# Performance work log

Hardware: AMD Instinct MI355X
Metric: run time of the kernel (lower is better)

## Reference

```python
import jax, jax.numpy as jnp
import numpy as np

N = 10000       # nodes
E = 200000      # node pairs (edges) in rel_dict
R = 400000      # relation instances
F_IN = 128
F_OUT = 64


def setup_inputs() -> dict:
    key = jax.random.key(0)
    ks = jax.random.split(key, 8)
    x = jax.random.normal(ks[0], (N, F_IN), dtype=jnp.float32)
    rel = jax.random.normal(ks[1], (R, F_IN), dtype=jnp.float32)
    adj = jax.random.uniform(ks[2], (N, N), dtype=jnp.float32)
    edge_pairs = jax.random.randint(ks[3], (E, 2), 0, N, dtype=jnp.int32)
    rel_seg = jax.random.randint(ks[4], (R,), 0, E, dtype=jnp.int32)
    # Conv1d(in, out, kernel_size=1, bias=False) == Linear: weight [out, in]
    W = jax.random.normal(ks[5], (F_OUT, F_IN), dtype=jnp.float32) * 0.1
    w_rel = jax.random.normal(ks[6], (F_IN,), dtype=jnp.float32) * 0.1
    bias = jnp.zeros((F_OUT,), dtype=jnp.float32)
    return {"x": x, "rel": rel, "adj": adj, "edge_pairs": edge_pairs,
            "rel_seg": rel_seg, "W": W, "w_rel": w_rel, "bias": bias}


def reference(x, rel, adj, edge_pairs, rel_seg, W, w_rel, bias):
    # node transform: [N, F_OUT]
    seq_fts = x @ W.T
    # per-relation scalar: [R]
    fts_rel = rel @ w_rel
    # segment-mean per edge (vectorized form of the rel_dict loop)
    sums = jax.ops.segment_sum(fts_rel, rel_seg, num_segments=E)
    cnts = jax.ops.segment_sum(jnp.ones_like(fts_rel), rel_seg, num_segments=E)
    edge_means = sums / jnp.maximum(cnts, 1.0)  # [E]
    # symmetric scatter into dense logits [N, N]
    e1, e2 = edge_pairs[:, 0], edge_pairs[:, 1]
    logits = jnp.zeros_like(adj)
    logits = logits.at[e1, e2].set(edge_means).at[e2, e1].set(edge_means)
    # masked-ish softmax over rows, then sparse-weighted aggregation
    coefs = jax.nn.softmax(jax.nn.sigmoid(logits) + adj, axis=1)  # [N, N]
    # dropout is a no-op in eval mode (training=False)
    ret = coefs @ seq_fts + bias  # [N, F_OUT]
    return jax.nn.elu(ret)        # concat=True
```

## Files before the change

kernel.cpp:

```cpp
#include <hip/hip_runtime.h>
#include <math.h>

#define NN   10000
#define EE   200000
#define RR   400000
#define FIN  128
#define FOUT 64
#define NK   10048

#define HASH_BITS 20
#define HSIZE (1u << HASH_BITS)
#define HMASK (HSIZE - 1u)
#define ROWCAP 256

typedef __bf16 bf16x8 __attribute__((ext_vector_type(8)));
typedef __bf16 bf16x4 __attribute__((ext_vector_type(4)));
typedef float  f32x4  __attribute__((ext_vector_type(4)));

#define O_SUMS   0
#define O_CNTS   (O_SUMS + EE)
#define O_ROWCNT (O_CNTS + EE)
#define O_HKEY   (O_ROWCNT + NN)
#define O_HPRIO  (O_HKEY + HSIZE)
#define O_SEQT   (O_HPRIO + HSIZE)
#define ZERO_WORDS (O_SEQT + (FOUT * NK) / 2)
#define O_SEQ    ZERO_WORDS
#define O_NUMP   (O_SEQ + NN * FOUT)
#define O_SP     (O_NUMP + 8 * NN * FOUT)
#define O_PAIRS  (O_SP + 8 * NN)

__global__ __launch_bounds__(256) void k_zero(f32x4* __restrict__ p, int n4) {
    int gid = blockIdx.x * 256 + threadIdx.x;
    if (gid < n4) p[gid] = (f32x4){0.f, 0.f, 0.f, 0.f};
}

__global__ __launch_bounds__(256) void k_seqfts(const float* __restrict__ x,
                                                const float* __restrict__ W,
                                                float* __restrict__ seq,
                                                __bf16* __restrict__ seqT) {
    __shared__ float Wt[FIN][FOUT + 1];
    __shared__ float xs[FIN][16 + 1];
    int t = threadIdx.x;
    for (int e = t; e < FOUT * FIN; e += 256) {
        int c = e >> 7, k = e & 127;
        Wt[k][c] = W[e];
    }
    int row0 = blockIdx.x * 16;
    for (int e = t; e < 16 * FIN; e += 256) {
        int r = e >> 7, k = e & 127;
        int gr = row0 + r;
        xs[k][r] = (gr < NN) ? x[(size_t)gr * FIN + k] : 0.f;
    }
    __syncthreads();
    int col = t & 63;
    int rg  = t >> 6;
    float acc[4] = {0.f, 0.f, 0.f, 0.f};
    for (int k = 0; k < FIN; ++k) {
        float w = Wt[k][col];
        #pragma unroll
        for (int i = 0; i < 4; ++i) acc[i] += w * xs[k][rg * 4 + i];
    }
    #pragma unroll
    for (int i = 0; i < 4; ++i) {
        int gr = row0 + rg * 4 + i;
        if (gr < NN) {
            seq[(size_t)gr * FOUT + col] = acc[i];
            seqT[(size_t)col * NK + gr] = (__bf16)acc[i];
        }
    }
}

__device__ __forceinline__ unsigned hash_cell(unsigned cell) {
    return (cell * 2654435761u) >> (32 - HASH_BITS);
}
__device__ __forceinline__ void entry_ij(const int* ep, int e, int& i, int& j, int& k) {
    k = (e < EE) ? e : e - EE;
    int a = ep[2 * k], b = ep[2 * k + 1];
    if (e < EE) { i = a; j = b; } else { i = b; j = a; }
}

#define BM 64
#define BK 64
#define KSPLIT 8
#define NCHUNK 157
#define CPK ((NCHUNK + KSPLIT - 1) / KSPLIT)
#define MAINB (NCHUNK * KSPLIT)
#define ILV   11
#define MRB   (ILV * MAINB)
#define SCATAB ((2 * EE + 255) / 256)
#define GRID_MR (MRB + SCATAB)
#define LDAP (BK + 8)

__global__ __launch_bounds__(256) void k_mainrel(const float* __restrict__ adj,
                                                 const __bf16* __restrict__ seqT,
                                                 const float* __restrict__ rel,
                                                 const float* __restrict__ wrel,
                                                 const int* __restrict__ rseg,
                                                 const int* __restrict__ ep,
                                                 float* __restrict__ sums,
                                                 float* __restrict__ cnts,
                                                 unsigned* __restrict__ hkey,
                                                 unsigned* __restrict__ hprio,
                                                 float* __restrict__ Nump,
                                                 float* __restrict__ Sp) {
    __shared__ __bf16 As[2][BM][LDAP];
    __shared__ __bf16 Bs[2][FOUT][LDAP];
    int t   = threadIdx.x;
    int bid = blockIdx.x;

    if (bid >= MRB) {
        int e = (bid - MRB) * 256 + t;
        if (e >= 2 * EE) return;
        int i, j, k;
        entry_ij(ep, e, i, j, k);
        unsigned cell = (unsigned)i * NN + (unsigned)j;
        unsigned keyv = cell + 1u;
        unsigned h = hash_cell(cell);
        while (true) {
            unsigned old = atomicCAS(&hkey[h], 0u, keyv);
            if (old == 0u || old == keyv) break;
            h = (h + 1u) & HMASK;
        }
        atomicMax(&hprio[h], (unsigned)(e + 1));
        return;
    }

    if (bid % ILV) {
        int relb = bid - bid / ILV - 1;
        int lane = t & 31;
        f32x4 w = *(const f32x4*)(wrel + lane * 4);
        #pragma unroll
        for (int it = 0; it < 4; ++it) {
            int row = relb * 32 + it * 8 + (t >> 5);
            if (row < RR) {
                f32x4 v = *(const f32x4*)(rel + (size_t)row * FIN + lane * 4);
                float s = v.x * w.x + v.y * w.y + v.z * w.z + v.w * w.w;
                #pragma unroll
                for (int off = 16; off >= 1; off >>= 1) s += __shfl_xor(s, off, 64);
                if (lane == 0) {
                    int seg = rseg[row];
                    atomicAdd(&sums[seg], s);
                    atomicAdd(&cnts[seg], 1.0f);
                }
            }
        }
        return;
    }

    int mi   = bid / ILV;
    int rowc = mi % NCHUNK;
    int ks   = mi / NCHUNK;
    int row0 = rowc * BM;
    int c0   = ks * CPK;
    int c1   = min(NCHUNK, c0 + CPK);
    int w  = t >> 6, l = t & 63;
    int lr = l & 15, lk = l >> 4;
    int sr = t >> 4;
    int sk = (t & 15) * 4;
    int bc = t >> 3;
    int bk = (t & 7) * 8;

    f32x4 acc[4];
    #pragma unroll
    for (int n = 0; n < 4; ++n) acc[n] = (f32x4){0.f, 0.f, 0.f, 0.f};
    float rs[4] = {0.f, 0.f, 0.f, 0.f};

    f32x4  pva[4];
    bf16x8 pvb0, pvb1;

#define LOADC(CH)                                                              \
    {                                                                          \
        int k0_ = (CH) * BK;                                                   \
        _Pragma("unroll")                                                      \
        for (int e2 = 0; e2 < 4; ++e2) {                                       \
            int gr = row0 + sr + e2 * 16;                                      \
            int gk = k0_ + sk;                                                 \
            bool ok = (gr < NN) && (gk < NN);                                  \
            pva[e2] = ok ? *(const f32x4*)(adj + (size_t)gr * NN + gk)         \
                         : (f32x4){0.f, 0.f, 0.f, 0.f};                        \
        }                                                                      \
        pvb0 = *(const bf16x8*)(seqT + (size_t)bc * NK + k0_ + bk);            \
        pvb1 = *(const bf16x8*)(seqT + (size_t)(bc + 32) * NK + k0_ + bk);     \
    }

    LOADC(c0);
    int p = 0;
    for (int ch = c0; ch < c1; ++ch) {
        *(bf16x8*)&Bs[p][bc][bk]      = pvb0;
        *(bf16x8*)&Bs[p][bc + 32][bk] = pvb1;
        bool okk = (ch * BK + sk < NN);
        #pragma unroll
        for (int e2 = 0; e2 < 4; ++e2) {
            bool ok = okk && (row0 + sr + e2 * 16 < NN);
            float w0 = ok ? __expf(pva[e2].x + 0.5f) : 0.f;
            float w1 = ok ? __expf(pva[e2].y + 0.5f) : 0.f;
            float w2 = ok ? __expf(pva[e2].z + 0.5f) : 0.f;
            float w3 = ok ? __expf(pva[e2].w + 0.5f) : 0.f;
            bf16x4 bv = { (__bf16)w0, (__bf16)w1, (__bf16)w2, (__bf16)w3 };
            *(bf16x4*)&As[p][sr + e2 * 16][sk] = bv;
            rs[e2] += w0 + w1 + w2 + w3;
        }
        if (ch + 1 < c1) LOADC(ch + 1);
        __syncthreads();
        #pragma unroll
        for (int kss = 0; kss < 2; ++kss) {
            bf16x8 a = *(const bf16x8*)&As[p][w * 16 + lr][kss * 32 + lk * 8];
            #pragma unroll
            for (int n = 0; n < 4; ++n) {
                bf16x8 b = *(const bf16x8*)&Bs[p][n * 16 + lr][kss * 32 + lk * 8];
                acc[n] = __builtin_amdgcn_mfma_f32_16x16x32_bf16(a, b, acc[n], 0, 0, 0);
            }
        }
        p ^= 1;
    }
#undef LOADC

    #pragma unroll
    for (int e = 0; e < 4; ++e) {
        float pp = rs[e];
        pp += __shfl_xor(pp, 1, 64);
        pp += __shfl_xor(pp, 2, 64);
        pp += __shfl_xor(pp, 4, 64);
        pp += __shfl_xor(pp, 8, 64);
        int r = e * 16 + sr;
        if ((t & 15) == 0 && row0 + r < NN)
            Sp[(size_t)ks * NN + row0 + r] = pp;
    }
    #pragma unroll
    for (int n = 0; n < 4; ++n) {
        #pragma unroll
        for (int r = 0; r < 4; ++r) {
            int grow = row0 + w * 16 + lk * 4 + r;
            if (grow < NN)
                Nump[(size_t)ks * NN * FOUT + (size_t)grow * FOUT + n * 16 + lr]
                    = acc[n][r];
        }
    }
}

__global__ __launch_bounds__(256) void k_scatB(const int* __restrict__ ep,
                                               const float* __restrict__ sums,
                                               const float* __restrict__ cnts,
                                               const unsigned* __restrict__ hkey,
                                               const unsigned* __restrict__ hprio,
                                               const float* __restrict__ adj,
                                               int* __restrict__ rowcnt,
                                               uint2* __restrict__ pairs) {
    int e = blockIdx.x * 256 + threadIdx.x;
    if (e >= 2 * EE) return;
    int i, j, k;
    entry_ij(ep, e, i, j, k);
    unsigned cell = (unsigned)i * NN + (unsigned)j;
    unsigned keyv = cell + 1u;
    unsigned h = hash_cell(cell);
    while (hkey[h] != keyv) h = (h + 1u) & HMASK;
    if (hprio[h] == (unsigned)(e + 1)) {
        float v   = sums[k] / fmaxf(cnts[k], 1.0f);
        float sg  = 1.f / (1.f + __expf(-v));
        float aij = adj[(size_t)i * NN + j];
        float dw  = __expf(aij + sg) - __expf(aij + 0.5f);
        if (dw != 0.f) {
            int pos = atomicAdd(&rowcnt[i], 1);
            if (pos < ROWCAP)
                pairs[(size_t)i * ROWCAP + pos] =
                    make_uint2((unsigned)j, __float_as_uint(dw));
        }
    }
}

__global__ __launch_bounds__(256) void k_rowupd(const float* __restrict__ Nump,
                                                const float* __restrict__ Sp,
                                                const int* __restrict__ rowcnt,
                                                const uint2* __restrict__ pairs,
                                                const float* __restrict__ seq,
                                                const float* __restrict__ bias,
                                                float* __restrict__ out) {
    int t = threadIdx.x;
    int i = blockIdx.x * 4 + (t >> 6);
    if (i >= NN) return;
    int c = t & 63;
    float acc = 0.f, sb = 0.f;
    #pragma unroll
    for (int ks = 0; ks < 8; ++ks) {
        acc += Nump[(size_t)ks * NN * FOUT + (size_t)i * FOUT + c];
        sb  += Sp[(size_t)ks * NN + i];
    }
    int cnt = min(rowcnt[i], ROWCAP);
    float sdw = 0.f;
    const uint2* pr = pairs + (size_t)i * ROWCAP;
    #pragma unroll 4
    for (int e = 0; e < cnt; ++e) {
        uint2 pk = pr[e];
        float d  = __uint_as_float(pk.y);
        acc += d * seq[(size_t)pk.x * FOUT + c];
        sdw += d;
    }
    float v = acc / (sb + sdw) + bias[c];
    out[(size_t)i * FOUT + c] = (v > 0.f) ? v : expm1f(v);
}

extern "C" void kernel_launch(void* const* d_in, const int* in_sizes, int n_in,
                              void* d_out, int out_size, void* d_ws, size_t ws_size,
                              hipStream_t stream) {
    const float* x    = (const float*)d_in[0];
    const float* rel  = (const float*)d_in[1];
    const float* adj  = (const float*)d_in[2];
    const int*   ep   = (const int*)d_in[3];
    const int*   rseg = (const int*)d_in[4];
    const float* W    = (const float*)d_in[5];
    const float* wrel = (const float*)d_in[6];
    const float* bias = (const float*)d_in[7];
    float* out = (float*)d_out;

    float* ws = (float*)d_ws;
    float*    sums   = ws + O_SUMS;
    float*    cnts   = ws + O_CNTS;
    int*      rowcnt = (int*)(ws + O_ROWCNT);
    unsigned* hkey   = (unsigned*)(ws + O_HKEY);
    unsigned* hprio  = (unsigned*)(ws + O_HPRIO);
    __bf16*   seqT   = (__bf16*)(ws + O_SEQT);
    float*    seq    = ws + O_SEQ;
    float*    Nump   = ws + O_NUMP;
    float*    Sp     = ws + O_SP;
    uint2*    pairs  = (uint2*)(ws + O_PAIRS);

    int n4 = ZERO_WORDS / 4;
    k_zero<<<(n4 + 255) / 256, 256, 0, stream>>>((f32x4*)d_ws, n4);
    k_seqfts<<<NN / 16, 256, 0, stream>>>(x, W, seq, seqT);
    k_mainrel<<<GRID_MR, 256, 0, stream>>>(adj, seqT, rel, wrel, rseg, ep,
                                           sums, cnts, hkey, hprio, Nump, Sp);
    k_scatB<<<SCATAB, 256, 0, stream>>>(ep, sums, cnts, hkey, hprio, adj,
                                        rowcnt, pairs);
    k_rowupd<<<(NN + 3) / 4, 256, 0, stream>>>(Nump, Sp, rowcnt, pairs,
                                               seq, bias, out);
}
```

Baseline: 268.7 us.

## Restructure fused main kernel to per-wave register-only MFMA strips without LDS

```diff
diff --git a/kernel.cpp b/kernel.cpp
--- a/kernel.cpp
+++ b/kernel.cpp
@@ -14,7 +14,6 @@
 #define ROWCAP 256
 
 typedef __bf16 bf16x8 __attribute__((ext_vector_type(8)));
-typedef __bf16 bf16x4 __attribute__((ext_vector_type(4)));
 typedef float  f32x4  __attribute__((ext_vector_type(4)));
 
 #define O_SUMS   0
@@ -79,37 +78,113 @@
     if (e < EE) { i = a; j = b; } else { i = b; j = a; }
 }
 
-#define BM 64
 #define BK 64
 #define KSPLIT 8
 #define NCHUNK 157
-#define CPK ((NCHUNK + KSPLIT - 1) / KSPLIT)
-#define MAINB (NCHUNK * KSPLIT)
-#define ILV   11
-#define MRB   (ILV * MAINB)
-#define SCATAB ((2 * EE + 255) / 256)
-#define GRID_MR (MRB + SCATAB)
-#define LDAP (BK + 8)
-
-__global__ __launch_bounds__(256) void k_mainrel(const float* __restrict__ adj,
-                                                 const __bf16* __restrict__ seqT,
-                                                 const float* __restrict__ rel,
-                                                 const float* __restrict__ wrel,
-                                                 const int* __restrict__ rseg,
-                                                 const int* __restrict__ ep,
-                                                 float* __restrict__ sums,
-                                                 float* __restrict__ cnts,
-                                                 unsigned* __restrict__ hkey,
-                                                 unsigned* __restrict__ hprio,
-                                                 float* __restrict__ Nump,
-                                                 float* __restrict__ Sp) {
-    __shared__ __bf16 As[2][BM][LDAP];
-    __shared__ __bf16 Bs[2][FOUT][LDAP];
+#define CPK 20
+#define NSTRIP (NN / 16)
+#define MAINW (NSTRIP * KSPLIT)
+#define RELW  (RR / 16)
+#define HASHW ((2 * EE + 63) / 64)
+#define TOTW  (MAINW + RELW + HASHW)
+#define GRID_MR ((TOTW + 3) / 4)
+
+__global__ __launch_bounds__(256, 4) void k_mainrel(const float* __restrict__ adj,
+                                                    const __bf16* __restrict__ seqT,
+                                                    const float* __restrict__ rel,
+                                                    const float* __restrict__ wrel,
+                                                    const int* __restrict__ rseg,
+                                                    const int* __restrict__ ep,
+                                                    float* __restrict__ sums,
+                                                    float* __restrict__ cnts,
+                                                    unsigned* __restrict__ hkey,
+                                                    unsigned* __restrict__ hprio,
+                                                    float* __restrict__ Nump,
+                                                    float* __restrict__ Sp) {
     int t   = threadIdx.x;
-    int bid = blockIdx.x;
-
-    if (bid >= MRB) {
-        int e = (bid - MRB) * 256 + t;
+    int wid = blockIdx.x * 4 + (t >> 6);
+    int l   = t & 63;
+
+    if (wid < MAINW) {
+        int strip = wid % NSTRIP;
+        int ks    = wid / NSTRIP;
+        int row0  = strip * 16;
+        int c0 = ks * CPK, c1 = min(NCHUNK, c0 + CPK);
+        int lr = l & 15, lk = l >> 4;
+        const float*  arow  = adj  + (size_t)(row0 + lr) * NN;
+        const __bf16* bbase = seqT + (size_t)lr * NK;
+
+        f32x4 acc[4];
+        #pragma unroll
+        for (int n = 0; n < 4; ++n) acc[n] = (f32x4){0.f, 0.f, 0.f, 0.f};
+        float rs = 0.f;
+
+        for (int ch = c0; ch < c1; ++ch) {
+            int k0 = ch * BK;
+            #pragma unroll
+            for (int h = 0; h < 2; ++h) {
+                int gk = k0 + h * 32 + lk * 8;
+                f32x4 a0 = (f32x4){-1e9f, -1e9f, -1e9f, -1e9f};
+                f32x4 a1 = a0;
+                if (gk < NN) {
+                    a0 = *(const f32x4*)(arow + gk);
+                    a1 = *(const f32x4*)(arow + gk + 4);
+                }
+                float w0 = __expf(a0.x + 0.5f);
+                float w1 = __expf(a0.y + 0.5f);
+                float w2 = __expf(a0.z + 0.5f);
+                float w3 = __expf(a0.w + 0.5f);
+                float w4 = __expf(a1.x + 0.5f);
+                float w5 = __expf(a1.y + 0.5f);
+                float w6 = __expf(a1.z + 0.5f);
+                float w7 = __expf(a1.w + 0.5f);
+                rs += ((w0 + w1) + (w2 + w3)) + ((w4 + w5) + (w6 + w7));
+                bf16x8 af = { (__bf16)w0, (__bf16)w1, (__bf16)w2, (__bf16)w3,
+                              (__bf16)w4, (__bf16)w5, (__bf16)w6, (__bf16)w7 };
+                const __bf16* bp = bbase + gk;
+                #pragma unroll
+                for (int n = 0; n < 4; ++n) {
+                    bf16x8 b = *(const bf16x8*)(bp + (size_t)n * 16 * NK);
+                    acc[n] = __builtin_amdgcn_mfma_f32_16x16x32_bf16(af, b, acc[n], 0, 0, 0);
+                }
+            }
+        }
+        rs += __shfl_xor(rs, 16, 64);
+        rs += __shfl_xor(rs, 32, 64);
+        if (lk == 0) Sp[(size_t)ks * NN + row0 + lr] = rs;
+        float* nout = Nump + (size_t)ks * NN * FOUT;
+        #pragma unroll
+        for (int n = 0; n < 4; ++n) {
+            #pragma unroll
+            for (int r = 0; r < 4; ++r)
+                nout[(size_t)(row0 + lk * 4 + r) * FOUT + n * 16 + lr] = acc[n][r];
+        }
+        return;
+    }
+
+    if (wid < MAINW + RELW) {
+        int rw   = wid - MAINW;
+        int lane = l & 31;
+        int half = l >> 5;
+        f32x4 wv = *(const f32x4*)(wrel + lane * 4);
+        #pragma unroll
+        for (int it = 0; it < 8; ++it) {
+            int row = rw * 16 + it * 2 + half;
+            f32x4 v = *(const f32x4*)(rel + (size_t)row * FIN + lane * 4);
+            float s = v.x * wv.x + v.y * wv.y + v.z * wv.z + v.w * wv.w;
+            #pragma unroll
+            for (int off = 16; off >= 1; off >>= 1) s += __shfl_xor(s, off, 64);
+            if (lane == 0) {
+                int seg = rseg[row];
+                atomicAdd(&sums[seg], s);
+                atomicAdd(&cnts[seg], 1.0f);
+            }
+        }
+        return;
+    }
+
+    {
+        int e = (wid - MAINW - RELW) * 64 + l;
         if (e >= 2 * EE) return;
         int i, j, k;
         entry_ij(ep, e, i, j, k);
@@ -122,119 +197,6 @@
             h = (h + 1u) & HMASK;
         }
         atomicMax(&hprio[h], (unsigned)(e + 1));
-        return;
-    }
-
-    if (bid % ILV) {
-        int relb = bid - bid / ILV - 1;
-        int lane = t & 31;
-        f32x4 w = *(const f32x4*)(wrel + lane * 4);
-        #pragma unroll
-        for (int it = 0; it < 4; ++it) {
-            int row = relb * 32 + it * 8 + (t >> 5);
-            if (row < RR) {
-                f32x4 v = *(const f32x4*)(rel + (size_t)row * FIN + lane * 4);
-                float s = v.x * w.x + v.y * w.y + v.z * w.z + v.w * w.w;
-                #pragma unroll
-                for (int off = 16; off >= 1; off >>= 1) s += __shfl_xor(s, off, 64);
-                if (lane == 0) {
-                    int seg = rseg[row];
-                    atomicAdd(&sums[seg], s);
-                    atomicAdd(&cnts[seg], 1.0f);
-                }
-            }
-        }
-        return;
-    }
-
-    int mi   = bid / ILV;
-    int rowc = mi % NCHUNK;
-    int ks   = mi / NCHUNK;
-    int row0 = rowc * BM;
-    int c0   = ks * CPK;
-    int c1   = min(NCHUNK, c0 + CPK);
-    int w  = t >> 6, l = t & 63;
-    int lr = l & 15, lk = l >> 4;
-    int sr = t >> 4;
-    int sk = (t & 15) * 4;
-    int bc = t >> 3;
-    int bk = (t & 7) * 8;
-
-    f32x4 acc[4];
-    #pragma unroll
-    for (int n = 0; n < 4; ++n) acc[n] = (f32x4){0.f, 0.f, 0.f, 0.f};
-    float rs[4] = {0.f, 0.f, 0.f, 0.f};
-
-    f32x4  pva[4];
-    bf16x8 pvb0, pvb1;
-
-#define LOADC(CH)                                                              \
-    {                                                                          \
-        int k0_ = (CH) * BK;                                                   \
-        _Pragma("unroll")                                                      \
-        for (int e2 = 0; e2 < 4; ++e2) {                                       \
-            int gr = row0 + sr + e2 * 16;                                      \
-            int gk = k0_ + sk;                                                 \
-            bool ok = (gr < NN) && (gk < NN);                                  \
-            pva[e2] = ok ? *(const f32x4*)(adj + (size_t)gr * NN + gk)         \
-                         : (f32x4){0.f, 0.f, 0.f, 0.f};                        \
-        }                                                                      \
-        pvb0 = *(const bf16x8*)(seqT + (size_t)bc * NK + k0_ + bk);            \
-        pvb1 = *(const bf16x8*)(seqT + (size_t)(bc + 32) * NK + k0_ + bk);     \
-    }
-
-    LOADC(c0);
-    int p = 0;
-    for (int ch = c0; ch < c1; ++ch) {
-        *(bf16x8*)&Bs[p][bc][bk]      = pvb0;
-        *(bf16x8*)&Bs[p][bc + 32][bk] = pvb1;
-        bool okk = (ch * BK + sk < NN);
-        #pragma unroll
-        for (int e2 = 0; e2 < 4; ++e2) {
-            bool ok = okk && (row0 + sr + e2 * 16 < NN);
-            float w0 = ok ? __expf(pva[e2].x + 0.5f) : 0.f;
-            float w1 = ok ? __expf(pva[e2].y + 0.5f) : 0.f;
-            float w2 = ok ? __expf(pva[e2].z + 0.5f) : 0.f;
-            float w3 = ok ? __expf(pva[e2].w + 0.5f) : 0.f;
-            bf16x4 bv = { (__bf16)w0, (__bf16)w1, (__bf16)w2, (__bf16)w3 };
-            *(bf16x4*)&As[p][sr + e2 * 16][sk] = bv;
-            rs[e2] += w0 + w1 + w2 + w3;
-        }
-        if (ch + 1 < c1) LOADC(ch + 1);
-        __syncthreads();
-        #pragma unroll
-        for (int kss = 0; kss < 2; ++kss) {
-            bf16x8 a = *(const bf16x8*)&As[p][w * 16 + lr][kss * 32 + lk * 8];
-            #pragma unroll
-            for (int n = 0; n < 4; ++n) {
-                bf16x8 b = *(const bf16x8*)&Bs[p][n * 16 + lr][kss * 32 + lk * 8];
-                acc[n] = __builtin_amdgcn_mfma_f32_16x16x32_bf16(a, b, acc[n], 0, 0, 0);
-            }
-        }
-        p ^= 1;
-    }
-#undef LOADC
-
-    #pragma unroll
-    for (int e = 0; e < 4; ++e) {
-        float pp = rs[e];
-        pp += __shfl_xor(pp, 1, 64);
-        pp += __shfl_xor(pp, 2, 64);
-        pp += __shfl_xor(pp, 4, 64);
-        pp += __shfl_xor(pp, 8, 64);
-        int r = e * 16 + sr;
-        if ((t & 15) == 0 && row0 + r < NN)
-            Sp[(size_t)ks * NN + row0 + r] = pp;
-    }
-    #pragma unroll
-    for (int n = 0; n < 4; ++n) {
-        #pragma unroll
-        for (int r = 0; r < 4; ++r) {
-            int grow = row0 + w * 16 + lk * 4 + r;
-            if (grow < NN)
-                Nump[(size_t)ks * NN * FOUT + (size_t)grow * FOUT + n * 16 + lr]
-                    = acc[n][r];
-        }
     }
 }
 
@@ -329,8 +291,8 @@
     k_seqfts<<<NN / 16, 256, 0, stream>>>(x, W, seq, seqT);
     k_mainrel<<<GRID_MR, 256, 0, stream>>>(adj, seqT, rel, wrel, rseg, ep,
                                            sums, cnts, hkey, hprio, Nump, Sp);
-    k_scatB<<<SCATAB, 256, 0, stream>>>(ep, sums, cnts, hkey, hprio, adj,
-                                        rowcnt, pairs);
+    k_scatB<<<(2 * EE + 255) / 256, 256, 0, stream>>>(ep, sums, cnts, hkey, hprio,
+                                                      adj, rowcnt, pairs);
     k_rowupd<<<(NN + 3) / 4, 256, 0, stream>>>(Nump, Sp, rowcnt, pairs,
                                                seq, bias, out);
 }
```

New measurement: 310.4 us. +15.5%, slower.

## Pre-pack seq features in MFMA fragment layout and fold row sums into MFMA

Applied to the files above, without the earlier changes.

```diff
diff --git a/kernel.cpp b/kernel.cpp
--- a/kernel.cpp
+++ b/kernel.cpp
@@ -6,12 +6,13 @@
 #define RR   400000
 #define FIN  128
 #define FOUT 64
-#define NK   10048
 
 #define HASH_BITS 20
 #define HSIZE (1u << HASH_BITS)
 #define HMASK (HSIZE - 1u)
 #define ROWCAP 256
+
+#define NKB 314
 
 typedef __bf16 bf16x8 __attribute__((ext_vector_type(8)));
 typedef __bf16 bf16x4 __attribute__((ext_vector_type(4)));
@@ -22,10 +23,10 @@
 #define O_ROWCNT (O_CNTS + EE)
 #define O_HKEY   (O_ROWCNT + NN)
 #define O_HPRIO  (O_HKEY + HSIZE)
-#define O_SEQT   (O_HPRIO + HSIZE)
-#define ZERO_WORDS (O_SEQT + (FOUT * NK) / 2)
-#define O_SEQ    ZERO_WORDS
-#define O_NUMP   (O_SEQ + NN * FOUT)
+#define O_SEQTP  (O_HPRIO + HSIZE)
+#define SEQTP_WORDS (NKB * 5 * 512 / 2)
+#define ZERO_WORDS (O_SEQTP + SEQTP_WORDS)
+#define O_NUMP   ZERO_WORDS
 #define O_SP     (O_NUMP + 8 * NN * FOUT)
 #define O_PAIRS  (O_SP + 8 * NN)
 
@@ -36,8 +37,7 @@
 
 __global__ __launch_bounds__(256) void k_seqfts(const float* __restrict__ x,
                                                 const float* __restrict__ W,
-                                                float* __restrict__ seq,
-                                                __bf16* __restrict__ seqT) {
+                                                __bf16* __restrict__ seqTp) {
     __shared__ float Wt[FIN][FOUT + 1];
     __shared__ float xs[FIN][16 + 1];
     int t = threadIdx.x;
@@ -63,10 +63,11 @@
     #pragma unroll
     for (int i = 0; i < 4; ++i) {
         int gr = row0 + rg * 4 + i;
-        if (gr < NN) {
-            seq[(size_t)gr * FOUT + col] = acc[i];
-            seqT[(size_t)col * NK + gr] = (__bf16)acc[i];
-        }
+        int kb = gr >> 5, g = (gr >> 3) & 3, slot = gr & 7;
+        seqTp[((size_t)kb * 5 + (col >> 4)) * 512 + ((col & 15) + g * 16) * 8 + slot]
+            = (__bf16)acc[i];
+        if (col < 16)
+            seqTp[((size_t)kb * 5 + 4) * 512 + (col + g * 16) * 8 + slot] = (__bf16)1.0f;
     }
 }
 
@@ -83,16 +84,16 @@
 #define BK 64
 #define KSPLIT 8
 #define NCHUNK 157
-#define CPK ((NCHUNK + KSPLIT - 1) / KSPLIT)
+#define CPK 20
 #define MAINB (NCHUNK * KSPLIT)
 #define ILV   11
 #define MRB   (ILV * MAINB)
 #define SCATAB ((2 * EE + 255) / 256)
 #define GRID_MR (MRB + SCATAB)
-#define LDAP (BK + 8)
+#define LDAP 72
 
 __global__ __launch_bounds__(256) void k_mainrel(const float* __restrict__ adj,
-                                                 const __bf16* __restrict__ seqT,
+                                                 const __bf16* __restrict__ seqTp,
                                                  const float* __restrict__ rel,
                                                  const float* __restrict__ wrel,
                                                  const int* __restrict__ rseg,
@@ -104,7 +105,6 @@
                                                  float* __restrict__ Nump,
                                                  float* __restrict__ Sp) {
     __shared__ __bf16 As[2][BM][LDAP];
-    __shared__ __bf16 Bs[2][FOUT][LDAP];
     int t   = threadIdx.x;
     int bid = blockIdx.x;
 
@@ -157,83 +157,95 @@
     int lr = l & 15, lk = l >> 4;
     int sr = t >> 4;
     int sk = (t & 15) * 4;
-    int bc = t >> 3;
-    int bk = (t & 7) * 8;
-
-    f32x4 acc[4];
+
+    f32x4 acc[5];
     #pragma unroll
-    for (int n = 0; n < 4; ++n) acc[n] = (f32x4){0.f, 0.f, 0.f, 0.f};
-    float rs[4] = {0.f, 0.f, 0.f, 0.f};
-
-    f32x4  pva[4];
-    bf16x8 pvb0, pvb1;
-
-#define LOADC(CH)                                                              \
+    for (int n = 0; n < 5; ++n) acc[n] = (f32x4){0.f, 0.f, 0.f, 0.f};
+
+    f32x4 pvA[4], pvB[4];
+
+#define LOADA(PV, CH)                                                          \
     {                                                                          \
         int k0_ = (CH) * BK;                                                   \
         _Pragma("unroll")                                                      \
         for (int e2 = 0; e2 < 4; ++e2) {                                       \
             int gr = row0 + sr + e2 * 16;                                      \
             int gk = k0_ + sk;                                                 \
-            bool ok = (gr < NN) && (gk < NN);                                  \
-            pva[e2] = ok ? *(const f32x4*)(adj + (size_t)gr * NN + gk)         \
-                         : (f32x4){0.f, 0.f, 0.f, 0.f};                        \
+            PV[e2] = (gr < NN && gk < NN)                                      \
+                         ? *(const f32x4*)(adj + (size_t)gr * NN + gk)         \
+                         : (f32x4){-1e9f, -1e9f, -1e9f, -1e9f};                \
         }                                                                      \
-        pvb0 = *(const bf16x8*)(seqT + (size_t)bc * NK + k0_ + bk);            \
-        pvb1 = *(const bf16x8*)(seqT + (size_t)(bc + 32) * NK + k0_ + bk);     \
-    }
-
-    LOADC(c0);
-    int p = 0;
-    for (int ch = c0; ch < c1; ++ch) {
-        *(bf16x8*)&Bs[p][bc][bk]      = pvb0;
-        *(bf16x8*)&Bs[p][bc + 32][bk] = pvb1;
-        bool okk = (ch * BK + sk < NN);
-        #pragma unroll
-        for (int e2 = 0; e2 < 4; ++e2) {
-            bool ok = okk && (row0 + sr + e2 * 16 < NN);
-            float w0 = ok ? __expf(pva[e2].x + 0.5f) : 0.f;
-            float w1 = ok ? __expf(pva[e2].y + 0.5f) : 0.f;
-            float w2 = ok ? __expf(pva[e2].z + 0.5f) : 0.f;
-            float w3 = ok ? __expf(pva[e2].w + 0.5f) : 0.f;
-            bf16x4 bv = { (__bf16)w0, (__bf16)w1, (__bf16)w2, (__bf16)w3 };
-            *(bf16x4*)&As[p][sr + e2 * 16][sk] = bv;
-            rs[e2] += w0 + w1 + w2 + w3;
-        }
-        if (ch + 1 < c1) LOADC(ch + 1);
-        __syncthreads();
-        #pragma unroll
-        for (int kss = 0; kss < 2; ++kss) {
-            bf16x8 a = *(const bf16x8*)&As[p][w * 16 + lr][kss * 32 + lk * 8];
-            #pragma unroll
-            for (int n = 0; n < 4; ++n) {
-                bf16x8 b = *(const bf16x8*)&Bs[p][n * 16 + lr][kss * 32 + lk * 8];
-                acc[n] = __builtin_amdgcn_mfma_f32_16x16x32_bf16(a, b, acc[n], 0, 0, 0);
-            }
-        }
-        p ^= 1;
-    }
-#undef LOADC
-
-    #pragma unroll
-    for (int e = 0; e < 4; ++e) {
-        float pp = rs[e];
-        pp += __shfl_xor(pp, 1, 64);
-        pp += __shfl_xor(pp, 2, 64);
-        pp += __shfl_xor(pp, 4, 64);
-        pp += __shfl_xor(pp, 8, 64);
-        int r = e * 16 + sr;
-        if ((t & 15) == 0 && row0 + r < NN)
-            Sp[(size_t)ks * NN + row0 + r] = pp;
-    }
+    }
+
+#define BODY(PV, CH, P_)                                                       \
+    {                                                                          \
+        _Pragma("unroll")                                                      \
+        for (int e2 = 0; e2 < 4; ++e2) {                                       \
+            f32x4 v = PV[e2];                                                  \
+            float e0 = exp2f(fmaf(v.x, 1.442695041f, 0.7213475204f));          \
+            float e1 = exp2f(fmaf(v.y, 1.442695041f, 0.7213475204f));          \
+            float e2f = exp2f(fmaf(v.z, 1.442695041f, 0.7213475204f));         \
+            float e3 = exp2f(fmaf(v.w, 1.442695041f, 0.7213475204f));          \
+            bf16x4 q = { (__bf16)e0, (__bf16)e1, (__bf16)e2f, (__bf16)e3 };    \
+            *(bf16x4*)&As[P_][sr + e2 * 16][sk] = q;                           \
+        }                                                                      \
+        const __bf16* bp = seqTp + (size_t)(CH) * 2 * 5 * 512 + l * 8;         \
+        bf16x8 b0 = *(const bf16x8*)(bp);                                      \
+        bf16x8 b1 = *(const bf16x8*)(bp + 512);                                \
+        bf16x8 b2 = *(const bf16x8*)(bp + 1024);                               \
+        bf16x8 b3 = *(const bf16x8*)(bp + 1536);                               \
+        bf16x8 b4 = *(const bf16x8*)(bp + 2048);                               \
+        __syncthreads();                                                       \
+        bf16x8 a0 = *(const bf16x8*)&As[P_][w * 16 + lr][lk * 8];              \
+        acc[0] = __builtin_amdgcn_mfma_f32_16x16x32_bf16(a0, b0, acc[0], 0, 0, 0); \
+        acc[1] = __builtin_amdgcn_mfma_f32_16x16x32_bf16(a0, b1, acc[1], 0, 0, 0); \
+        acc[2] = __builtin_amdgcn_mfma_f32_16x16x32_bf16(a0, b2, acc[2], 0, 0, 0); \
+        acc[3] = __builtin_amdgcn_mfma_f32_16x16x32_bf16(a0, b3, acc[3], 0, 0, 0); \
+        acc[4] = __builtin_amdgcn_mfma_f32_16x16x32_bf16(a0, b4, acc[4], 0, 0, 0); \
+        const __bf16* bq = bp + 2560;                                          \
+        bf16x8 d0 = *(const bf16x8*)(bq);                                      \
+        bf16x8 d1 = *(const bf16x8*)(bq + 512);                                \
+        bf16x8 d2 = *(const bf16x8*)(bq + 1024);                               \
+        bf16x8 d3 = *(const bf16x8*)(bq + 1536);                               \
+        bf16x8 d4 = *(const bf16x8*)(bq + 2048);                               \
+        bf16x8 a1 = *(const bf16x8*)&As[P_][w * 16 + lr][32 + lk * 8];         \
+        acc[0] = __builtin_amdgcn_mfma_f32_16x16x32_bf16(a1, d0, acc[0], 0, 0, 0); \
+        acc[1] = __builtin_amdgcn_mfma_f32_16x16x32_bf16(a1, d1, acc[1], 0, 0, 0); \
+        acc[2] = __builtin_amdgcn_mfma_f32_16x16x32_bf16(a1, d2, acc[2], 0, 0, 0); \
+        acc[3] = __builtin_amdgcn_mfma_f32_16x16x32_bf16(a1, d3, acc[3], 0, 0, 0); \
+        acc[4] = __builtin_amdgcn_mfma_f32_16x16x32_bf16(a1, d4, acc[4], 0, 0, 0); \
+    }
+
+    LOADA(pvA, c0);
+    int ch = c0, p = 0;
+    while (true) {
+        if (ch + 1 < c1) LOADA(pvB, ch + 1);
+        BODY(pvA, ch, p);
+        p ^= 1; ++ch;
+        if (ch >= c1) break;
+        if (ch + 1 < c1) LOADA(pvA, ch + 1);
+        BODY(pvB, ch, p);
+        p ^= 1; ++ch;
+        if (ch >= c1) break;
+    }
+#undef LOADA
+#undef BODY
+
+    float* nout = Nump + (size_t)ks * NN * FOUT;
     #pragma unroll
     for (int n = 0; n < 4; ++n) {
         #pragma unroll
         for (int r = 0; r < 4; ++r) {
             int grow = row0 + w * 16 + lk * 4 + r;
             if (grow < NN)
-                Nump[(size_t)ks * NN * FOUT + (size_t)grow * FOUT + n * 16 + lr]
-                    = acc[n][r];
+                nout[(size_t)grow * FOUT + n * 16 + lr] = acc[n][r];
+        }
+    }
+    if (lr == 0) {
+        #pragma unroll
+        for (int r = 0; r < 4; ++r) {
+            int grow = row0 + w * 16 + lk * 4 + r;
+            if (grow < NN) Sp[(size_t)ks * NN + grow] = acc[4][r];
         }
     }
 }
@@ -272,7 +284,7 @@
                                                 const float* __restrict__ Sp,
                                                 const int* __restrict__ rowcnt,
                                                 const uint2* __restrict__ pairs,
-                                                const float* __restrict__ seq,
+                                                const __bf16* __restrict__ seqTp,
                                                 const float* __restrict__ bias,
                                                 float* __restrict__ out) {
     int t = threadIdx.x;
@@ -288,11 +300,13 @@
     int cnt = min(rowcnt[i], ROWCAP);
     float sdw = 0.f;
     const uint2* pr = pairs + (size_t)i * ROWCAP;
-    #pragma unroll 4
     for (int e = 0; e < cnt; ++e) {
         uint2 pk = pr[e];
         float d  = __uint_as_float(pk.y);
-        acc += d * seq[(size_t)pk.x * FOUT + c];
+        unsigned j = pk.x;
+        float sj = (float)seqTp[((size_t)(j >> 5) * 5 + (c >> 4)) * 512
+                                + ((c & 15) + ((j >> 3) & 3) * 16) * 8 + (j & 7)];
+        acc += d * sj;
         sdw += d;
     }
     float v = acc / (sb + sdw) + bias[c];
@@ -318,19 +332,18 @@
     int*      rowcnt = (int*)(ws + O_ROWCNT);
     unsigned* hkey   = (unsigned*)(ws + O_HKEY);
     unsigned* hprio  = (unsigned*)(ws + O_HPRIO);
-    __bf16*   seqT   = (__bf16*)(ws + O_SEQT);
-    float*    seq    = ws + O_SEQ;
+    __bf16*   seqTp  = (__bf16*)(ws + O_SEQTP);
     float*    Nump   = ws + O_NUMP;
     float*    Sp     = ws + O_SP;
     uint2*    pairs  = (uint2*)(ws + O_PAIRS);
 
     int n4 = ZERO_WORDS / 4;
     k_zero<<<(n4 + 255) / 256, 256, 0, stream>>>((f32x4*)d_ws, n4);
-    k_seqfts<<<NN / 16, 256, 0, stream>>>(x, W, seq, seqT);
-    k_mainrel<<<GRID_MR, 256, 0, stream>>>(adj, seqT, rel, wrel, rseg, ep,
+    k_seqfts<<<NN / 16, 256, 0, stream>>>(x, W, seqTp);
+    k_mainrel<<<GRID_MR, 256, 0, stream>>>(adj, seqTp, rel, wrel, rseg, ep,
                                            sums, cnts, hkey, hprio, Nump, Sp);
-    k_scatB<<<SCATAB, 256, 0, stream>>>(ep, sums, cnts, hkey, hprio, adj,
-                                        rowcnt, pairs);
+    k_scatB<<<(2 * EE + 255) / 256, 256, 0, stream>>>(ep, sums, cnts, hkey, hprio,
+                                                      adj, rowcnt, pairs);
     k_rowupd<<<(NN + 3) / 4, 256, 0, stream>>>(Nump, Sp, rowcnt, pairs,
-                                               seq, bias, out);
-}
+                                               seqTp, bias, out);
+}
```

New measurement: 319.7 us. 19.0% more time.
